# Kernel optimization log

Hardware: AMD Instinct MI355X
Metric: run time of the kernel (lower is better)

Reference implementation:

```python
import jax, jax.numpy as jnp
import numpy as np

EPS = 1e-8
INPUT, HIDDEN, OUTPUT = 128, 256, 64
BATCH, SEQ = 2048, 512


def _normalize(v):
    return v / (jnp.linalg.norm(v, axis=-1, keepdims=True) + EPS)


def _col_normalize(w):
    # matches torch init: divide by column norms (norm over dim=0)
    return w / (jnp.linalg.norm(w, axis=0, keepdims=True) + EPS)


def setup_inputs() -> dict:
    key = jax.random.key(0)
    ks = jax.random.split(key, 9)
    x = jax.random.normal(ks[0], (BATCH, SEQ, INPUT), dtype=jnp.float32)
    h_init = _normalize(jax.random.normal(ks[1], (BATCH, HIDDEN), dtype=jnp.float32))
    input_weights = _col_normalize(jax.random.normal(ks[2], (INPUT, HIDDEN), dtype=jnp.float32))
    recurrent_weights = _col_normalize(jax.random.normal(ks[3], (HIDDEN, HIDDEN), dtype=jnp.float32))
    output_weights = _col_normalize(jax.random.normal(ks[4], (HIDDEN, OUTPUT), dtype=jnp.float32))
    lambda_i = jax.random.normal(ks[5], (HIDDEN,), dtype=jnp.float32)
    lambda_r = jax.random.normal(ks[6], (HIDDEN,), dtype=jnp.float32)
    s_z = jax.random.normal(ks[7], (1,), dtype=jnp.float32)
    alpha_raw = jax.random.normal(ks[8], (HIDDEN,), dtype=jnp.float32)
    return {
        'x': x, 'h_init': h_init,
        'input_weights': input_weights,
        'recurrent_weights': recurrent_weights,
        'output_weights': output_weights,
        'lambda_i': lambda_i, 'lambda_r': lambda_r,
        's_z': s_z, 'alpha_raw': alpha_raw,
    }


def reference(x, h_init, input_weights, recurrent_weights, output_weights,
              lambda_i, lambda_r, s_z, alpha_raw):
    # NLNN forward (eval mode: dropout is identity).
    alpha = jax.nn.sigmoid(alpha_raw)  # [H]

    def slerp(h_t, h_new):
        h_t = _normalize(h_t)
        h_new = _normalize(h_new)
        dot = jnp.sum(h_t * h_new, axis=-1, keepdims=True)  # [B,1]
        dot = jnp.clip(dot, -1.0 + EPS, 1.0 - EPS)
        theta = jnp.arccos(dot)
        sin_theta = jnp.sin(theta)
        mask = (sin_theta > EPS).astype(h_t.dtype)
        c_t = jnp.sin((1.0 - alpha) * theta) / (sin_theta + EPS)   # [B,H]
        c_n = jnp.sin(alpha * theta) / (sin_theta + EPS)           # [B,H]
        res = mask * (c_t * h_t + c_n * h_new) + (1.0 - mask) * h_new
        return _normalize(res)

    def step(h_t, x_t):
        input_proj = lambda_i * (x_t @ input_weights)        # [B,H]
        recurrent_proj = lambda_r * (h_t @ recurrent_weights)  # [B,H]
        h_new = _normalize(input_proj + recurrent_proj)
        h_t = slerp(h_t, h_new)
        out = s_z * (h_t @ output_weights)                    # [B,O]
        return h_t, out

    h_fin, outs = jax.lax.scan(step, h_init, jnp.swapaxes(x, 0, 1))  # outs: [S,B,O]
    return jnp.swapaxes(outs, 0, 1), h_fin
```

## Files before the change

kernel.cpp:

```cpp
#include <hip/hip_runtime.h>
#include <stdint.h>

#define SEQ    512
#define IN_D   128
#define HID    256
#define OUT_D  64

typedef __attribute__((ext_vector_type(8))) short bf16x8;
typedef __attribute__((ext_vector_type(4))) float f32x4;

__device__ __forceinline__ uint16_t f2bf(float f) {
  union { float f; uint32_t u; } v; v.f = f;
  uint32_t r = v.u + 0x7FFFu + ((v.u >> 16) & 1u);
  return (uint16_t)(r >> 16);
}
__device__ __forceinline__ uint32_t packbf(float a, float b) {
  return (uint32_t)f2bf(a) | ((uint32_t)f2bf(b) << 16);
}

__global__ __launch_bounds__(512, 2) void nlnn_kernel(
    const float* __restrict__ x, const float* __restrict__ h0,
    const float* __restrict__ Win, const float* __restrict__ Wrec,
    const float* __restrict__ Wout, const float* __restrict__ lami,
    const float* __restrict__ lamr, const float* __restrict__ szp,
    const float* __restrict__ araw, float* __restrict__ out) {

  __shared__ __align__(16) short lds_ax[2][16 * 136];
  __shared__ __align__(16) short lds_ah[16 * 264];
  __shared__ __align__(16) float lds_hnew[8 * 256];

  const int tid = threadIdx.x;
  const int w   = tid >> 6;
  const int l   = tid & 63;
  const int l15 = l & 15;
  const int q   = l >> 4;
  const int blk = blockIdx.x;
  const int row_g = blk * 8 + w;

  bf16x8 wb[12][2];
#pragma unroll
  for (int nt = 0; nt < 2; ++nt) {
    const int col = 32 * w + 16 * nt + l15;
    const float li = lami[col], lr = lamr[col];
#pragma unroll
    for (int kt = 0; kt < 12; ++kt) {
#pragma unroll
      for (int i = 0; i < 8; ++i) {
        const int k = 32 * kt + 8 * q + i;
        const float v = (k < IN_D) ? li * Win[k * HID + col]
                                   : lr * Wrec[(k - IN_D) * HID + col];
        wb[kt][nt][i] = (short)f2bf(v);
      }
    }
  }
  bf16x8 wo[8];
  {
    const float sz = szp[0];
    const int col = 16 * (w & 3) + l15;
#pragma unroll
    for (int kt = 0; kt < 8; ++kt)
#pragma unroll
      for (int i = 0; i < 8; ++i) {
        const int k = 32 * kt + 8 * q + i;
        wo[kt][i] = (short)f2bf(sz * Wout[k * OUT_D + col]);
      }
  }

  float al[4];
#pragma unroll
  for (int i = 0; i < 4; ++i)
    al[i] = 1.0f / (1.0f + expf(-araw[4 * l + i]));

  float hc[4];
  {
    const f32x4 h4 = *(const f32x4*)&h0[(size_t)row_g * HID + 4 * l];
    hc[0] = h4.x; hc[1] = h4.y; hc[2] = h4.z; hc[3] = h4.w;
    *(uint32_t*)&lds_ah[w * 264 + 4 * l]     = packbf(hc[0], hc[1]);
    *(uint32_t*)&lds_ah[w * 264 + 4 * l + 2] = packbf(hc[2], hc[3]);
  }
  {
    const float2 xv = *(const float2*)&x[(size_t)row_g * (SEQ * IN_D) + 2 * l];
    *(uint32_t*)&lds_ax[0][w * 136 + 2 * l] = packbf(xv.x, xv.y);
  }
  __syncthreads();

  for (int t = 0; t < SEQ; ++t) {
    const int p = t & 1;
    const int tn = (t + 1 < SEQ) ? t + 1 : SEQ - 1;
    const float2 xv = *(const float2*)&x[((size_t)row_g * SEQ + tn) * IN_D + 2 * l];

    f32x4 acc0 = {0.f, 0.f, 0.f, 0.f};
    f32x4 acc1 = {0.f, 0.f, 0.f, 0.f};
    const short* ax = &lds_ax[p][l15 * 136 + 8 * q];
    const short* ah = &lds_ah[l15 * 264 + 8 * q];
#pragma unroll
    for (int kt = 0; kt < 4; ++kt) {
      bf16x8 a = *(const bf16x8*)(ax + 32 * kt);
      acc0 = __builtin_amdgcn_mfma_f32_16x16x32_bf16(a, wb[kt][0], acc0, 0, 0, 0);
      acc1 = __builtin_amdgcn_mfma_f32_16x16x32_bf16(a, wb[kt][1], acc1, 0, 0, 0);
    }
#pragma unroll
    for (int kt = 0; kt < 8; ++kt) {
      bf16x8 a = *(const bf16x8*)(ah + 32 * kt);
      acc0 = __builtin_amdgcn_mfma_f32_16x16x32_bf16(a, wb[4 + kt][0], acc0, 0, 0, 0);
      acc1 = __builtin_amdgcn_mfma_f32_16x16x32_bf16(a, wb[4 + kt][1], acc1, 0, 0, 0);
    }
    if (l < 32) {
      const int colb = 32 * w + l15;
      const int r0 = 4 * q;
#pragma unroll
      for (int i = 0; i < 4; ++i) {
        lds_hnew[(r0 + i) * HID + colb]      = acc0[i];
        lds_hnew[(r0 + i) * HID + colb + 16] = acc1[i];
      }
    }
    *(uint32_t*)&lds_ax[p ^ 1][w * 136 + 2 * l] = packbf(xv.x, xv.y);
    __syncthreads();

    const f32x4 hn4 = *(const f32x4*)&lds_hnew[w * HID + 4 * l];
    float hn[4] = {hn4.x, hn4.y, hn4.z, hn4.w};
    float ss = hn[0]*hn[0] + hn[1]*hn[1] + hn[2]*hn[2] + hn[3]*hn[3];
    float dt = hc[0]*hn[0] + hc[1]*hn[1] + hc[2]*hn[2] + hc[3]*hn[3];
#pragma unroll
    for (int off = 32; off >= 1; off >>= 1) {
      ss += __shfl_xor(ss, off, 64);
      dt += __shfl_xor(dt, off, 64);
    }
    const float invn = 1.0f / (sqrtf(ss) + 1e-8f);
    float d = dt * invn;
    d = fminf(fmaxf(d, -1.0f), 1.0f);
    const float th = acosf(d);
    const float st = __sinf(th);
    const bool msk = st > 1e-8f;
    const float den = 1.0f / (st + 1e-8f);
    float res[4]; float ss2 = 0.f;
#pragma unroll
    for (int i = 0; i < 4; ++i) {
      const float hni = hn[i] * invn;
      const float ct = __sinf((1.0f - al[i]) * th) * den;
      const float cn = __sinf(al[i] * th) * den;
      const float r = msk ? (ct * hc[i] + cn * hni) : hni;
      res[i] = r; ss2 += r * r;
    }
#pragma unroll
    for (int off = 32; off >= 1; off >>= 1) ss2 += __shfl_xor(ss2, off, 64);
    const float inv2 = 1.0f / (sqrtf(ss2) + 1e-8f);
#pragma unroll
    for (int i = 0; i < 4; ++i) hc[i] = res[i] * inv2;
    *(uint32_t*)&lds_ah[w * 264 + 4 * l]     = packbf(hc[0], hc[1]);
    *(uint32_t*)&lds_ah[w * 264 + 4 * l + 2] = packbf(hc[2], hc[3]);
    __syncthreads();

    if (w < 4) {
      f32x4 ao = {0.f, 0.f, 0.f, 0.f};
      const short* ah2 = &lds_ah[l15 * 264 + 8 * q];
#pragma unroll
      for (int kt = 0; kt < 8; ++kt) {
        bf16x8 a = *(const bf16x8*)(ah2 + 32 * kt);
        ao = __builtin_amdgcn_mfma_f32_16x16x32_bf16(a, wo[kt], ao, 0, 0, 0);
      }
      if (l < 32) {
        const int col = 16 * w + l15;
        const int r0 = 4 * q;
#pragma unroll
        for (int i = 0; i < 4; ++i)
          out[((size_t)(blk * 8 + r0 + i) * SEQ + t) * OUT_D + col] = ao[i];
      }
    }
  }

  float* hf = out + (size_t)2048 * SEQ * OUT_D;
  f32x4 hv; hv.x = hc[0]; hv.y = hc[1]; hv.z = hc[2]; hv.w = hc[3];
  *(f32x4*)&hf[(size_t)row_g * HID + 4 * l] = hv;
}

extern "C" void kernel_launch(void* const* d_in, const int* in_sizes, int n_in,
                              void* d_out, int out_size, void* d_ws, size_t ws_size,
                              hipStream_t stream) {
  const float* x    = (const float*)d_in[0];
  const float* h0   = (const float*)d_in[1];
  const float* Win  = (const float*)d_in[2];
  const float* Wrec = (const float*)d_in[3];
  const float* Wout = (const float*)d_in[4];
  const float* li   = (const float*)d_in[5];
  const float* lr   = (const float*)d_in[6];
  const float* sz   = (const float*)d_in[7];
  const float* ar   = (const float*)d_in[8];
  nlnn_kernel<<<256, 512, 0, stream>>>(x, h0, Win, Wrec, Wout, li, lr, sz, ar,
                                       (float*)d_out);
}
```

Measured before the change: 1.719 ms.

## Defer output projection into next step and use DPP reductions with fast acos

Each step's output projection now reuses the h fragments already loaded for the recurrent matmul and is computed one step late. This removes a barrier and a second LDS read pass, and a final epilogue emits the last timestep. The x prefetch is moved two steps ahead, and the shuffle-based wave reductions are replaced by DPP row operations plus readlane. acosf is replaced by a polynomial approximation, and a custom barrier only waits on LDS counters. The changes trade some accuracy in theta for shorter serial latency per timestep.

```diff
diff --git a/kernel.cpp b/kernel.cpp
--- a/kernel.cpp
+++ b/kernel.cpp
@@ -16,6 +16,41 @@
 }
 __device__ __forceinline__ uint32_t packbf(float a, float b) {
   return (uint32_t)f2bf(a) | ((uint32_t)f2bf(b) << 16);
+}
+
+__device__ __forceinline__ float wave_sum(float x) {
+  x += __int_as_float(__builtin_amdgcn_update_dpp(0, __float_as_int(x), 0xB1, 0xF, 0xF, true));
+  x += __int_as_float(__builtin_amdgcn_update_dpp(0, __float_as_int(x), 0x4E, 0xF, 0xF, true));
+  x += __int_as_float(__builtin_amdgcn_update_dpp(0, __float_as_int(x), 0x124, 0xF, 0xF, true));
+  x += __int_as_float(__builtin_amdgcn_update_dpp(0, __float_as_int(x), 0x128, 0xF, 0xF, true));
+  const int xi = __float_as_int(x);
+  const float s0 = __int_as_float(__builtin_amdgcn_readlane(xi, 0));
+  const float s1 = __int_as_float(__builtin_amdgcn_readlane(xi, 16));
+  const float s2 = __int_as_float(__builtin_amdgcn_readlane(xi, 32));
+  const float s3 = __int_as_float(__builtin_amdgcn_readlane(xi, 48));
+  return (s0 + s1) + (s2 + s3);
+}
+
+__device__ __forceinline__ float fast_acos(float x) {
+  const float ax = fabsf(x);
+  float p = -0.0012624911f;
+  p = p * ax + 0.0066700901f;
+  p = p * ax - 0.0170881256f;
+  p = p * ax + 0.0308918810f;
+  p = p * ax - 0.0501743046f;
+  p = p * ax + 0.0889789874f;
+  p = p * ax - 0.2145988016f;
+  p = p * ax + 1.5707963050f;
+  p *= sqrtf(1.0f - ax);
+  return (x >= 0.0f) ? p : (3.14159265358979f - p);
+}
+
+__device__ __forceinline__ void lds_barrier() {
+  __builtin_amdgcn_sched_barrier(0);
+  asm volatile("s_waitcnt lgkmcnt(0)" ::: "memory");
+  __builtin_amdgcn_s_barrier();
+  asm volatile("" ::: "memory");
+  __builtin_amdgcn_sched_barrier(0);
 }
 
 __global__ __launch_bounds__(512, 2) void nlnn_kernel(
@@ -82,12 +117,17 @@
     const float2 xv = *(const float2*)&x[(size_t)row_g * (SEQ * IN_D) + 2 * l];
     *(uint32_t*)&lds_ax[0][w * 136 + 2 * l] = packbf(xv.x, xv.y);
   }
-  __syncthreads();
+  float2 xn = *(const float2*)&x[((size_t)row_g * SEQ + 1) * IN_D + 2 * l];
+  lds_barrier();
 
   for (int t = 0; t < SEQ; ++t) {
     const int p = t & 1;
-    const int tn = (t + 1 < SEQ) ? t + 1 : SEQ - 1;
-    const float2 xv = *(const float2*)&x[((size_t)row_g * SEQ + tn) * IN_D + 2 * l];
+
+    *(uint32_t*)&lds_ax[p ^ 1][w * 136 + 2 * l] = packbf(xn.x, xn.y);
+    {
+      const int tn = (t + 2 < SEQ) ? t + 2 : SEQ - 1;
+      xn = *(const float2*)&x[((size_t)row_g * SEQ + tn) * IN_D + 2 * l];
+    }
 
     f32x4 acc0 = {0.f, 0.f, 0.f, 0.f};
     f32x4 acc1 = {0.f, 0.f, 0.f, 0.f};
@@ -99,11 +139,12 @@
       acc0 = __builtin_amdgcn_mfma_f32_16x16x32_bf16(a, wb[kt][0], acc0, 0, 0, 0);
       acc1 = __builtin_amdgcn_mfma_f32_16x16x32_bf16(a, wb[kt][1], acc1, 0, 0, 0);
     }
+    bf16x8 af[8];
 #pragma unroll
     for (int kt = 0; kt < 8; ++kt) {
-      bf16x8 a = *(const bf16x8*)(ah + 32 * kt);
-      acc0 = __builtin_amdgcn_mfma_f32_16x16x32_bf16(a, wb[4 + kt][0], acc0, 0, 0, 0);
-      acc1 = __builtin_amdgcn_mfma_f32_16x16x32_bf16(a, wb[4 + kt][1], acc1, 0, 0, 0);
+      af[kt] = *(const bf16x8*)(ah + 32 * kt);
+      acc0 = __builtin_amdgcn_mfma_f32_16x16x32_bf16(af[kt], wb[4 + kt][0], acc0, 0, 0, 0);
+      acc1 = __builtin_amdgcn_mfma_f32_16x16x32_bf16(af[kt], wb[4 + kt][1], acc1, 0, 0, 0);
     }
     if (l < 32) {
       const int colb = 32 * w + l15;
@@ -114,58 +155,66 @@
         lds_hnew[(r0 + i) * HID + colb + 16] = acc1[i];
       }
     }
-    *(uint32_t*)&lds_ax[p ^ 1][w * 136 + 2 * l] = packbf(xv.x, xv.y);
-    __syncthreads();
+    if (w < 4) {
+      f32x4 ao = {0.f, 0.f, 0.f, 0.f};
+#pragma unroll
+      for (int kt = 0; kt < 8; ++kt)
+        ao = __builtin_amdgcn_mfma_f32_16x16x32_bf16(af[kt], wo[kt], ao, 0, 0, 0);
+      if (t > 0 && l < 32) {
+        const int col = 16 * w + l15;
+        const int r0 = 4 * q;
+#pragma unroll
+        for (int i = 0; i < 4; ++i)
+          out[((size_t)(blk * 8 + r0 + i) * SEQ + (t - 1)) * OUT_D + col] = ao[i];
+      }
+    }
+    lds_barrier();
 
     const f32x4 hn4 = *(const f32x4*)&lds_hnew[w * HID + 4 * l];
     float hn[4] = {hn4.x, hn4.y, hn4.z, hn4.w};
-    float ss = hn[0]*hn[0] + hn[1]*hn[1] + hn[2]*hn[2] + hn[3]*hn[3];
-    float dt = hc[0]*hn[0] + hc[1]*hn[1] + hc[2]*hn[2] + hc[3]*hn[3];
-#pragma unroll
-    for (int off = 32; off >= 1; off >>= 1) {
-      ss += __shfl_xor(ss, off, 64);
-      dt += __shfl_xor(dt, off, 64);
-    }
+    float ssp = hn[0]*hn[0] + hn[1]*hn[1] + hn[2]*hn[2] + hn[3]*hn[3];
+    float dtp = hc[0]*hn[0] + hc[1]*hn[1] + hc[2]*hn[2] + hc[3]*hn[3];
+    const float ss = wave_sum(ssp);
+    const float dtt = wave_sum(dtp);
     const float invn = 1.0f / (sqrtf(ss) + 1e-8f);
-    float d = dt * invn;
+    float d = dtt * invn;
     d = fminf(fmaxf(d, -1.0f), 1.0f);
-    const float th = acosf(d);
+    const float th = fast_acos(d);
     const float st = __sinf(th);
     const bool msk = st > 1e-8f;
     const float den = 1.0f / (st + 1e-8f);
-    float res[4]; float ss2 = 0.f;
+    float res[4]; float s2p = 0.f;
 #pragma unroll
     for (int i = 0; i < 4; ++i) {
       const float hni = hn[i] * invn;
       const float ct = __sinf((1.0f - al[i]) * th) * den;
       const float cn = __sinf(al[i] * th) * den;
       const float r = msk ? (ct * hc[i] + cn * hni) : hni;
-      res[i] = r; ss2 += r * r;
-    }
-#pragma unroll
-    for (int off = 32; off >= 1; off >>= 1) ss2 += __shfl_xor(ss2, off, 64);
-    const float inv2 = 1.0f / (sqrtf(ss2) + 1e-8f);
+      res[i] = r; s2p += r * r;
+    }
+    const float s2 = wave_sum(s2p);
+    const float inv2 = 1.0f / (sqrtf(s2) + 1e-8f);
 #pragma unroll
     for (int i = 0; i < 4; ++i) hc[i] = res[i] * inv2;
     *(uint32_t*)&lds_ah[w * 264 + 4 * l]     = packbf(hc[0], hc[1]);
     *(uint32_t*)&lds_ah[w * 264 + 4 * l + 2] = packbf(hc[2], hc[3]);
-    __syncthreads();
-
-    if (w < 4) {
-      f32x4 ao = {0.f, 0.f, 0.f, 0.f};
-      const short* ah2 = &lds_ah[l15 * 264 + 8 * q];
-#pragma unroll
-      for (int kt = 0; kt < 8; ++kt) {
-        bf16x8 a = *(const bf16x8*)(ah2 + 32 * kt);
-        ao = __builtin_amdgcn_mfma_f32_16x16x32_bf16(a, wo[kt], ao, 0, 0, 0);
-      }
-      if (l < 32) {
-        const int col = 16 * w + l15;
-        const int r0 = 4 * q;
-#pragma unroll
-        for (int i = 0; i < 4; ++i)
-          out[((size_t)(blk * 8 + r0 + i) * SEQ + t) * OUT_D + col] = ao[i];
-      }
+    lds_barrier();
+  }
+
+  if (w < 4) {
+    f32x4 ao = {0.f, 0.f, 0.f, 0.f};
+    const short* ah2 = &lds_ah[l15 * 264 + 8 * q];
+#pragma unroll
+    for (int kt = 0; kt < 8; ++kt) {
+      bf16x8 a = *(const bf16x8*)(ah2 + 32 * kt);
+      ao = __builtin_amdgcn_mfma_f32_16x16x32_bf16(a, wo[kt], ao, 0, 0, 0);
+    }
+    if (l < 32) {
+      const int col = 16 * w + l15;
+      const int r0 = 4 * q;
+#pragma unroll
+      for (int i = 0; i < 4; ++i)
+        out[((size_t)(blk * 8 + r0 + i) * SEQ + (SEQ - 1)) * OUT_D + col] = ao[i];
     }
   }
 
```

New measurement: 1.404 ms. 1.22x faster.
